# Optimization experiments

Measured on AMD Instinct MI355X. Metric: run time of the kernel, lower is better.

The kernel has to match this reference:

```python
import jax, jax.numpy as jnp
import numpy as np

PRED, TOTAL, ITEM = 100000, 120000, 100000
NUI = PRED + ITEM            # nodes in user2item / reverse-consumption graphs
NODES = TOTAL + ITEM         # embedding table rows
EMB = 64
EPS = 1e-5


def _gatv2(src, dst, x, Wl, bl, Wr, br, attn, n):
    """DGL GATv2Conv (1 head), activation=leaky_relu(0.01)."""
    fs = x @ Wl + bl                                   # fc_src
    fd = x @ Wr + br                                   # fc_dst
    e = jax.nn.leaky_relu(fs[src] + fd[dst], 0.2) @ attn   # [E_edges]
    m = jax.ops.segment_max(e, dst, n)                 # per-dst max (stable softmax)
    ex = jnp.exp(e - m[dst])
    denom = jax.ops.segment_sum(ex, dst, n)
    alpha = ex / denom[dst]                            # edge softmax over in-edges
    out = jax.ops.segment_sum(alpha[:, None] * fs[src], dst, n)
    return jax.nn.leaky_relu(out, 0.01)


def _bn(x, g, b):
    mu = jnp.mean(x, 0)
    var = jnp.var(x, 0)
    return (x - mu) * jax.lax.rsqrt(var + EPS) * g + b


def _mlp(x, W, b, g, beta):
    # Linear -> BatchNorm1d (train mode, batch stats) -> LeakyReLU(0.01)
    return jax.nn.leaky_relu(_bn(x @ W + b, g, beta), 0.01)


def _cheb(src, dst, x, W, b, lam, n):
    """ChebConv order-3: h = sum_k T_k(Lhat) x @ W_k + b, leaky_relu."""
    deg = jnp.clip(jax.ops.segment_sum(jnp.ones_like(dst, jnp.float32), dst, n), 1.0)
    dinv = jax.lax.rsqrt(deg)
    norm = dinv[src] * dinv[dst]                       # D^-1/2 A D^-1/2 edge weight

    def lhat(v):  # (2/lam)(I - Ahat) v - v
        av = jax.ops.segment_sum(norm[:, None] * v[src], dst, n)
        return (2.0 / lam) * (v - av) - v

    T0 = x
    T1 = lhat(T0)
    T2 = 2.0 * lhat(T1) - T0
    return jax.nn.leaky_relu(T0 @ W[0] + T1 @ W[1] + T2 @ W[2] + b, 0.01)


def setup_inputs() -> dict:
    key = jax.random.key(0)
    ks = jax.random.split(key, 24)
    ri = lambda k, n, hi: jax.random.randint(k, (n,), 0, hi, dtype=jnp.int32)
    rn = lambda k, shp, s=0.1: jax.random.normal(k, shp, jnp.float32) * s
    return {
        "emb": rn(ks[0], (NODES, EMB), 1.0),
        "bn0_g": jnp.ones((EMB,), jnp.float32),
        "bn0_b": jnp.zeros((EMB,), jnp.float32),
        "gat_Wl": rn(ks[1], (5, EMB, EMB)),
        "gat_bl": jnp.zeros((5, EMB), jnp.float32),
        "gat_Wr": rn(ks[2], (5, EMB, EMB)),
        "gat_br": jnp.zeros((5, EMB), jnp.float32),
        "gat_attn": rn(ks[3], (5, EMB)),
        "cheb_W": rn(ks[4], (3, EMB, EMB)),
        "cheb_b": jnp.zeros((EMB,), jnp.float32),
        "mlp_W": rn(ks[5], (5, 2 * EMB, EMB)),
        "mlp_b": jnp.zeros((5, EMB), jnp.float32),
        "mlp_g": jnp.ones((5, EMB), jnp.float32),
        "mlp_beta": jnp.zeros((5, EMB), jnp.float32),
        "lambda_max": jnp.array([2.0], jnp.float32),
        "u2i_src": ri(ks[6], 1500000, NUI),
        "u2i_dst": ri(ks[7], 1500000, NUI),
        "rc_src": ri(ks[8], 1500000, NUI),
        "rc_dst": ri(ks[9], 1500000, NUI),
        "i2u_src": ri(ks[10], 1000000, PRED),
        "i2u_dst": ri(ks[11], 1000000, PRED),
        "i2u_ids": jnp.arange(PRED, dtype=jnp.int32),
        "sn_src": ri(ks[12], 1000000, PRED),
        "sn_dst": ri(ks[13], 1000000, PRED),
        "snn_src": ri(ks[14], 1500000, TOTAL),
        "snn_dst": ri(ks[15], 1500000, TOTAL),
    }


def reference(emb, bn0_g, bn0_b, gat_Wl, gat_bl, gat_Wr, gat_br, gat_attn,
              cheb_W, cheb_b, mlp_W, mlp_b, mlp_g, mlp_beta, lambda_max,
              u2i_src, u2i_dst, rc_src, rc_dst, i2u_src, i2u_dst, i2u_ids,
              sn_src, sn_dst, snn_src, snn_dst):
    gat = lambda i, src, dst, x, n: _gatv2(src, dst, x, gat_Wl[i], gat_bl[i],
                                           gat_Wr[i], gat_br[i], gat_attn[i], n)
    mlp = lambda i, x: _mlp(x, mlp_W[i], mlp_b[i], mlp_g[i], mlp_beta[i])

    e = _bn(emb, bn0_g, bn0_b)                        # embedding_BN over all nodes
    pred_u = e[:PRED]
    total_u = e[:TOTAL]
    item_e = e[-ITEM:]
    uie = jnp.concatenate([pred_u, item_e], axis=0)   # [NUI, EMB]

    # --- spatial attention: item influence branch ---
    u2i_emb = gat(0, u2i_src, u2i_dst, uie, NUI)
    iie = gat(1, rc_src, rc_dst, u2i_emb, NUI)[:PRED]

    # --- spatial attention: social item branch ---
    su = uie[i2u_ids]                                 # embedding[_ID]
    i2u_emb = gat(2, i2u_src, i2u_dst, su, PRED)
    soc = uie[:PRED]                                  # embedding[social_g.nodes()]
    mask = (jnp.sum(i2u_emb, axis=1) != 0)[:, None]
    soc = soc.at[i2u_ids].set(jnp.where(mask, i2u_emb, soc[i2u_ids]))
    sie = gat(3, sn_src, sn_dst, soc, PRED)

    user_item_embed = mlp(0, jnp.concatenate([iie, sie], axis=1))

    # --- spectral attention ---
    lam = lambda_max[0]
    h = _cheb(snn_src, snn_dst, total_u, cheb_W, cheb_b, lam, TOTAL)
    h = _cheb(snn_src, snn_dst, h, cheb_W, cheb_b, lam, TOTAL)
    user_social_embed = gat(4, snn_src, snn_dst, h, TOTAL)[:PRED]

    # --- mutualistic layer ---
    h_uP = mlp(1, jnp.concatenate([user_item_embed, pred_u], axis=1))
    h_uS = mlp(2, jnp.concatenate([user_social_embed, pred_u], axis=1))
    h_m = h_uP * h_uS
    h_mP = jnp.concatenate([h_m * jax.nn.softmax(h_uP, axis=1), h_uP], axis=1)
    h_mS = jnp.concatenate([h_m * jax.nn.softmax(h_uS, axis=1), h_uS], axis=1)

    # --- prediction layer ---
    h_new_P = mlp(3, h_mP)
    h_new_S = mlp(4, h_mS)
    return (h_new_P, h_new_S)
```

## Files before the change

kernel.cpp:

```cpp
#include <hip/hip_runtime.h>
#include <math.h>

static const int PRED  = 100000;
static const int TOTAL = 120000;
static const int ITEM  = 100000;
static const int NUI   = PRED + ITEM;
static const int NODES = TOTAL + ITEM;
#define BN_EPS 1e-5f

__device__ inline float lrelu(float v, float s) { return v > 0.f ? v : s * v; }

__global__ void k_bn_stats(const float* __restrict__ x, int n, float* __restrict__ sums) {
  __shared__ float ls[256], ls2[256];
  int t = threadIdx.x;
  int col = t & 63;
  float s = 0.f, s2 = 0.f;
  for (int r = blockIdx.x * 4 + (t >> 6); r < n; r += gridDim.x * 4) {
    float v = x[(size_t)r * 64 + col];
    s += v; s2 += v * v;
  }
  ls[t] = s; ls2[t] = s2;
  __syncthreads();
  if (t < 64) {
    atomicAdd(&sums[t],      ls[t] + ls[t + 64] + ls[t + 128] + ls[t + 192]);
    atomicAdd(&sums[64 + t], ls2[t] + ls2[t + 64] + ls2[t + 128] + ls2[t + 192]);
  }
}

__global__ void k_bn_apply(const float* __restrict__ x, float* __restrict__ y,
                           const float* __restrict__ sums,
                           const float* __restrict__ g, const float* __restrict__ b,
                           int n, int relu) {
  size_t tot4 = (size_t)n * 16;
  size_t i = (size_t)blockIdx.x * blockDim.x + threadIdx.x;
  size_t st = (size_t)gridDim.x * blockDim.x;
  float inv_n = 1.f / (float)n;
  const float4* x4 = (const float4*)x;
  float4* y4 = (float4*)y;
  for (; i < tot4; i += st) {
    int c4 = (int)(i & 15) * 4;
    float4 v = x4[i];
    float4 o;
    #pragma unroll
    for (int j = 0; j < 4; ++j) {
      int c = c4 + j;
      float mean = sums[c] * inv_n;
      float var = fmaxf(sums[64 + c] * inv_n - mean * mean, 0.f);
      float vv = (j == 0) ? v.x : (j == 1) ? v.y : (j == 2) ? v.z : v.w;
      float oo = (vv - mean) * rsqrtf(var + BN_EPS) * g[c] + b[c];
      if (relu) oo = lrelu(oo, 0.01f);
      if (j == 0) o.x = oo; else if (j == 1) o.y = oo; else if (j == 2) o.z = oo; else o.w = oo;
    }
    y4[i] = o;
  }
}

__global__ void k_bn0_apply(const float* __restrict__ x, float* __restrict__ e_tot,
                            float* __restrict__ uie, const float* __restrict__ sums,
                            const float* __restrict__ g, const float* __restrict__ b) {
  size_t tot4 = (size_t)NODES * 16;
  size_t i = (size_t)blockIdx.x * blockDim.x + threadIdx.x;
  size_t st = (size_t)gridDim.x * blockDim.x;
  float inv_n = 1.f / (float)NODES;
  const float4* x4 = (const float4*)x;
  float4* e4 = (float4*)e_tot;
  float4* u4 = (float4*)uie;
  for (; i < tot4; i += st) {
    int c4 = (int)(i & 15) * 4;
    size_t row = i >> 4;
    float4 v = x4[i];
    float4 o;
    #pragma unroll
    for (int j = 0; j < 4; ++j) {
      int c = c4 + j;
      float mean = sums[c] * inv_n;
      float var = fmaxf(sums[64 + c] * inv_n - mean * mean, 0.f);
      float vv = (j == 0) ? v.x : (j == 1) ? v.y : (j == 2) ? v.z : v.w;
      float oo = (vv - mean) * rsqrtf(var + BN_EPS) * g[c] + b[c];
      if (j == 0) o.x = oo; else if (j == 1) o.y = oo; else if (j == 2) o.z = oo; else o.w = oo;
    }
    if (row < (size_t)TOTAL) e4[i] = o;
    else u4[((row - TOTAL) + PRED) * 16 + (i & 15)] = o;
    if (row < (size_t)PRED) u4[i] = o;
  }
}

__global__ __launch_bounds__(256) void k_gemm_dual(const float* __restrict__ A,
    const float* __restrict__ Wl, const float* __restrict__ bl,
    const float* __restrict__ Wr, const float* __restrict__ br,
    float* __restrict__ FS, float* __restrict__ FD, int n) {
  __shared__ float As[128][65];
  __shared__ float Ws[64][68];
  int t = threadIdx.x;
  int row0 = blockIdx.x * 128;
  for (int i = t; i < 2048; i += 256) {
    int r = i >> 4, c = (i & 15) * 4, gr = row0 + r;
    float4 a;
    if (gr < n) a = *(const float4*)&A[(size_t)gr * 64 + c];
    else { a.x = a.y = a.z = a.w = 0.f; }
    As[r][c] = a.x; As[r][c + 1] = a.y; As[r][c + 2] = a.z; As[r][c + 3] = a.w;
  }
  int cg = (t & 7) * 8;
  int rg = (t >> 3) * 4;
  for (int s = 0; s < 2; ++s) {
    const float* Wm = s ? Wr : Wl;
    const float* bias = s ? br : bl;
    __syncthreads();
    for (int i = t; i < 4096; i += 256) Ws[i >> 6][i & 63] = Wm[i];
    __syncthreads();
    float bb[8];
    *(float4*)&bb[0] = *(const float4*)&bias[cg];
    *(float4*)&bb[4] = *(const float4*)&bias[cg + 4];
    float acc[4][8];
    #pragma unroll
    for (int i = 0; i < 4; ++i)
      #pragma unroll
      for (int j = 0; j < 8; ++j) acc[i][j] = bb[j];
    for (int k = 0; k < 64; ++k) {
      float w[8], a[4];
      *(float4*)&w[0] = *(const float4*)&Ws[k][cg];
      *(float4*)&w[4] = *(const float4*)&Ws[k][cg + 4];
      #pragma unroll
      for (int i = 0; i < 4; ++i) a[i] = As[rg + i][k];
      #pragma unroll
      for (int i = 0; i < 4; ++i)
        #pragma unroll
        for (int j = 0; j < 8; ++j)
          acc[i][j] += a[i] * w[j];
    }
    float* C = s ? FD : FS;
    #pragma unroll
    for (int i = 0; i < 4; ++i) {
      int gr = row0 + rg + i;
      if (gr < n) {
        float4 o0, o1;
        o0.x = acc[i][0]; o0.y = acc[i][1]; o0.z = acc[i][2]; o0.w = acc[i][3];
        o1.x = acc[i][4]; o1.y = acc[i][5]; o1.z = acc[i][6]; o1.w = acc[i][7];
        *(float4*)&FS[0];
        *(float4*)&C[(size_t)gr * 64 + cg] = o0;
        *(float4*)&C[(size_t)gr * 64 + cg + 4] = o1;
      }
    }
  }
}

__global__ __launch_bounds__(256) void k_gemm_cat(const float* __restrict__ A1,
    const float* __restrict__ A2, const float* __restrict__ A3,
    const float* __restrict__ Wm, const float* __restrict__ bias,
    float* __restrict__ C, int n, int nseg, int relu, float* __restrict__ stats) {
  __shared__ float As[128][65];
  __shared__ float Ws[64][68];
  __shared__ float st[128];
  int t = threadIdx.x;
  int row0 = blockIdx.x * 128;
  int cg = (t & 7) * 8;
  int rg = (t >> 3) * 4;
  float bb[8];
  *(float4*)&bb[0] = *(const float4*)&bias[cg];
  *(float4*)&bb[4] = *(const float4*)&bias[cg + 4];
  float acc[4][8];
  #pragma unroll
  for (int i = 0; i < 4; ++i)
    #pragma unroll
    for (int j = 0; j < 8; ++j) acc[i][j] = bb[j];
  for (int s = 0; s < nseg; ++s) {
    const float* A = (s == 0) ? A1 : (s == 1) ? A2 : A3;
    __syncthreads();
    for (int i = t; i < 4096; i += 256) Ws[i >> 6][i & 63] = Wm[s * 4096 + i];
    for (int i = t; i < 2048; i += 256) {
      int r = i >> 4, c = (i & 15) * 4, gr = row0 + r;
      float4 a;
      if (gr < n) a = *(const float4*)&A[(size_t)gr * 64 + c];
      else { a.x = a.y = a.z = a.w = 0.f; }
      As[r][c] = a.x; As[r][c + 1] = a.y; As[r][c + 2] = a.z; As[r][c + 3] = a.w;
    }
    __syncthreads();
    for (int k = 0; k < 64; ++k) {
      float w[8], a[4];
      *(float4*)&w[0] = *(const float4*)&Ws[k][cg];
      *(float4*)&w[4] = *(const float4*)&Ws[k][cg + 4];
      #pragma unroll
      for (int i = 0; i < 4; ++i) a[i] = As[rg + i][k];
      #pragma unroll
      for (int i = 0; i < 4; ++i)
        #pragma unroll
        for (int j = 0; j < 8; ++j)
          acc[i][j] += a[i] * w[j];
    }
  }
  float csum[8], csq[8];
  #pragma unroll
  for (int j = 0; j < 8; ++j) { csum[j] = 0.f; csq[j] = 0.f; }
  #pragma unroll
  for (int i = 0; i < 4; ++i) {
    int gr = row0 + rg + i;
    if (gr < n) {
      #pragma unroll
      for (int j = 0; j < 8; ++j) {
        float o = acc[i][j];
        if (relu) o = lrelu(o, 0.01f);
        acc[i][j] = o;
        csum[j] += o;
        csq[j] += o * o;
      }
      float4 o0, o1;
      o0.x = acc[i][0]; o0.y = acc[i][1]; o0.z = acc[i][2]; o0.w = acc[i][3];
      o1.x = acc[i][4]; o1.y = acc[i][5]; o1.z = acc[i][6]; o1.w = acc[i][7];
      *(float4*)&C[(size_t)gr * 64 + cg] = o0;
      *(float4*)&C[(size_t)gr * 64 + cg + 4] = o1;
    }
  }
  if (stats) {
    __syncthreads();
    if (t < 128) st[t] = 0.f;
    __syncthreads();
    #pragma unroll
    for (int j = 0; j < 8; ++j) {
      atomicAdd(&st[cg + j], csum[j]);
      atomicAdd(&st[64 + cg + j], csq[j]);
    }
    __syncthreads();
    if (t < 128) atomicAdd(&stats[t], st[t]);
  }
}

__global__ __launch_bounds__(512) void k_bhist(const int* __restrict__ dst, int* __restrict__ M,
                                               int E, int nbuck, int chunk) {
  __shared__ int h[1600];
  int t = threadIdx.x, b = blockIdx.x;
  for (int k = t; k < nbuck; k += 512) h[k] = 0;
  __syncthreads();
  int beg = b * chunk, end = min(E, beg + chunk);
  for (int i = beg + t; i < end; i += 512) atomicAdd(&h[dst[i] >> 7], 1);
  __syncthreads();
  for (int k = t; k < nbuck; k += 512) M[k * 64 + b] = h[k];
}

__global__ void k_scan_part(const int* __restrict__ counts, int* __restrict__ bsums, int n) {
  __shared__ int sh[256];
  int t = threadIdx.x;
  int i = blockIdx.x * 256 + t;
  sh[t] = (i < n) ? counts[i] : 0;
  __syncthreads();
  for (int o = 128; o; o >>= 1) {
    if (t < o) sh[t] += sh[t + o];
    __syncthreads();
  }
  if (t == 0) bsums[blockIdx.x] = sh[0];
}

__global__ void k_scan_tops(int* __restrict__ bsums, int nb) {
  __shared__ int sh[256];
  int t = threadIdx.x;
  int carry = 0;
  for (int base = 0; base < nb; base += 256) {
    int i = base + t;
    int v = (i < nb) ? bsums[i] : 0;
    __syncthreads();
    sh[t] = v;
    __syncthreads();
    for (int o = 1; o < 256; o <<= 1) {
      int tv = (t >= o) ? sh[t - o] : 0;
      __syncthreads();
      sh[t] += tv;
      __syncthreads();
    }
    int incl = sh[t];
    int total = sh[255];
    if (i < nb) bsums[i] = incl - v + carry;
    carry += total;
  }
}

__global__ void k_scan_apply_ip(int* __restrict__ cnts, const int* __restrict__ bsums, int n) {
  __shared__ int sh[256];
  int t = threadIdx.x;
  int i = blockIdx.x * 256 + t;
  int v = (i < n) ? cnts[i] : 0;
  sh[t] = v;
  __syncthreads();
  for (int o = 1; o < 256; o <<= 1) {
    int tv = (t >= o) ? sh[t - o] : 0;
    __syncthreads();
    sh[t] += tv;
    __syncthreads();
  }
  if (i < n) cnts[i] = sh[t] - v + bsums[blockIdx.x];
}

__global__ __launch_bounds__(512) void k_bscatter(const int* __restrict__ src, const int* __restrict__ dst,
                                                  const int* __restrict__ M, unsigned int* __restrict__ tmp,
                                                  int E, int nbuck, int chunk) {
  __shared__ int cur[1600];
  int t = threadIdx.x, b = blockIdx.x;
  for (int k = t; k < nbuck; k += 512) cur[k] = M[k * 64 + b];
  __syncthreads();
  int beg = b * chunk, end = min(E, beg + chunk);
  for (int i = beg + t; i < end; i += 512) {
    int d = dst[i];
    int pos = atomicAdd(&cur[d >> 7], 1);
    tmp[pos] = ((unsigned int)(d & 127) << 25) | (unsigned int)src[i];
  }
}

__global__ __launch_bounds__(256) void k_bfinal(const unsigned int* __restrict__ tmp,
                                                const int* __restrict__ M,
                                                int* __restrict__ offs, int* __restrict__ csr,
                                                int E, int nbuck, int n,
                                                float* __restrict__ dinvOut) {
  __shared__ int h[128];
  int t = threadIdx.x, k = blockIdx.x;
  int base = M[k * 64];
  int next = (k + 1 < nbuck) ? M[(k + 1) * 64] : E;
  if (t < 128) h[t] = 0;
  __syncthreads();
  for (int i = base + t; i < next; i += 256) atomicAdd(&h[tmp[i] >> 25], 1);
  __syncthreads();
  if (t == 0) { int s = 0; for (int j = 0; j < 128; ++j) { int c = h[j]; h[j] = s; s += c; } }
  __syncthreads();
  int r0 = k << 7;
  int hstart = 0, hnext = 0;
  if (t < 128) {
    hstart = h[t];
    hnext = (t < 127) ? h[t + 1] : (next - base);
  }
  if (t < 128 && r0 + t < n) {
    offs[r0 + t] = base + hstart;
    if (dinvOut) dinvOut[r0 + t] = rsqrtf(fmaxf((float)(hnext - hstart), 1.f));
  }
  if (k == nbuck - 1 && t == 0) offs[n] = E;
  __syncthreads();
  for (int i = base + t; i < next; i += 256) {
    unsigned int v = tmp[i];
    int rl = (int)(v >> 25);
    int pos = base + atomicAdd(&h[rl], 1);
    csr[pos] = (int)(v & 0x01FFFFFFu);
  }
}

__global__ __launch_bounds__(256) void k_gat_fused(const float* __restrict__ fs,
                                                   const float* __restrict__ fd,
                                                   const float* __restrict__ attn,
                                                   const int* __restrict__ offs,
                                                   const int* __restrict__ csr_src,
                                                   const float* __restrict__ sel,
                                                   float* __restrict__ out, int n) {
  int lane = threadIdx.x & 63;
  int g  = lane >> 4;
  int li = lane & 15;
  int c4 = li * 4;
  int wid = (blockIdx.x * blockDim.x + threadIdx.x) >> 6;
  int nw = (gridDim.x * blockDim.x) >> 6;
  float4 ak = *(const float4*)&attn[c4];
  for (int r = wid; r < n; r += nw) {
    int beg = offs[r], end = offs[r + 1];
    float4 fdv = *(const float4*)&fd[(size_t)r * 64 + c4];
    float den = 0.f;
    float4 acc; acc.x = acc.y = acc.z = acc.w = 0.f;
    int e0 = beg + g;
    int s = (e0 < end) ? csr_src[e0] : 0;
    float4 f = *(const float4*)&fs[(size_t)s * 64 + c4];
    for (int e4 = beg; e4 < end; e4 += 4) {
      bool act = (e4 + g) < end;
      int en = e4 + 4 + g;
      int sn = (en < end) ? csr_src[en] : 0;
      float4 fn = *(const float4*)&fs[(size_t)sn * 64 + c4];
      float w = ak.x * lrelu(f.x + fdv.x, 0.2f)
              + ak.y * lrelu(f.y + fdv.y, 0.2f)
              + ak.z * lrelu(f.z + fdv.z, 0.2f)
              + ak.w * lrelu(f.w + fdv.w, 0.2f);
      w += __shfl_xor(w, 1);
      w += __shfl_xor(w, 2);
      w += __shfl_xor(w, 4);
      w += __shfl_xor(w, 8);
      float p = act ? __expf(w) : 0.f;
      den += p;
      acc.x += p * f.x;
      acc.y += p * f.y;
      acc.z += p * f.z;
      acc.w += p * f.w;
      s = sn; f = fn;
    }
    #pragma unroll
    for (int o = 16; o < 64; o <<= 1) {
      den   += __shfl_xor(den, o);
      acc.x += __shfl_xor(acc.x, o);
      acc.y += __shfl_xor(acc.y, o);
      acc.z += __shfl_xor(acc.z, o);
      acc.w += __shfl_xor(acc.w, o);
    }
    if (g == 0) {
      float inv = (end > beg) ? 1.f / den : 0.f;
      float4 o4;
      o4.x = lrelu(acc.x * inv, 0.01f);
      o4.y = lrelu(acc.y * inv, 0.01f);
      o4.z = lrelu(acc.z * inv, 0.01f);
      o4.w = lrelu(acc.w * inv, 0.01f);
      if (sel) {
        float rs = o4.x + o4.y + o4.z + o4.w;
        rs += __shfl_xor(rs, 1);
        rs += __shfl_xor(rs, 2);
        rs += __shfl_xor(rs, 4);
        rs += __shfl_xor(rs, 8);
        if (rs == 0.f) o4 = *(const float4*)&sel[(size_t)r * 64 + c4];
      }
      *(float4*)&out[(size_t)r * 64 + c4] = o4;
    }
  }
}

__global__ __launch_bounds__(256) void k_cheb_fused(const float* __restrict__ v,
                                                    const float* __restrict__ t0,
                                                    const float* __restrict__ dinv,
                                                    const int* __restrict__ offs,
                                                    const int* __restrict__ csr_src,
                                                    float* __restrict__ out,
                                                    const float* __restrict__ lamf,
                                                    int n, int mode) {
  int lane = threadIdx.x & 63;
  int g  = lane >> 4;
  int li = lane & 15;
  int c4 = li * 4;
  int wid = (blockIdx.x * blockDim.x + threadIdx.x) >> 6;
  int nw = (gridDim.x * blockDim.x) >> 6;
  float cc = 2.f / lamf[0];
  for (int r = wid; r < n; r += nw) {
    int beg = offs[r], end = offs[r + 1];
    float dr = dinv[r];
    float4 acc; acc.x = acc.y = acc.z = acc.w = 0.f;
    int e0 = beg + g;
    int s = (e0 < end) ? csr_src[e0] : 0;
    float ds = dinv[s];
    float4 f = *(const float4*)&v[(size_t)s * 64 + c4];
    for (int e4 = beg; e4 < end; e4 += 4) {
      bool act = (e4 + g) < end;
      int en = e4 + 4 + g;
      int sn = (en < end) ? csr_src[en] : 0;
      float dsn = dinv[sn];
      float4 fn = *(const float4*)&v[(size_t)sn * 64 + c4];
      float ns = act ? ds * dr : 0.f;
      acc.x += ns * f.x;
      acc.y += ns * f.y;
      acc.z += ns * f.z;
      acc.w += ns * f.w;
      s = sn; ds = dsn; f = fn;
    }
    #pragma unroll
    for (int o = 16; o < 64; o <<= 1) {
      acc.x += __shfl_xor(acc.x, o);
      acc.y += __shfl_xor(acc.y, o);
      acc.z += __shfl_xor(acc.z, o);
      acc.w += __shfl_xor(acc.w, o);
    }
    if (g == 0) {
      float4 vr = *(const float4*)&v[(size_t)r * 64 + c4];
      float4 o4;
      o4.x = cc * (vr.x - acc.x) - vr.x;
      o4.y = cc * (vr.y - acc.y) - vr.y;
      o4.z = cc * (vr.z - acc.z) - vr.z;
      o4.w = cc * (vr.w - acc.w) - vr.w;
      if (mode == 2) {
        float4 t = *(const float4*)&t0[(size_t)r * 64 + c4];
        o4.x = 2.f * o4.x - t.x;
        o4.y = 2.f * o4.y - t.y;
        o4.z = 2.f * o4.z - t.z;
        o4.w = 2.f * o4.w - t.w;
      }
      *(float4*)&out[(size_t)r * 64 + c4] = o4;
    }
  }
}

__global__ void k_softmax_mul(const float* __restrict__ a, const float* __restrict__ b,
                              float* __restrict__ out, int n) {
  int lane = threadIdx.x & 63;
  int wid = (blockIdx.x * blockDim.x + threadIdx.x) >> 6;
  int nw = (gridDim.x * blockDim.x) >> 6;
  for (int r = wid; r < n; r += nw) {
    size_t idx = (size_t)r * 64 + lane;
    float av = a[idx];
    float mx = av;
    for (int o = 32; o; o >>= 1) mx = fmaxf(mx, __shfl_xor(mx, o));
    float e = expf(av - mx);
    float s = e;
    for (int o = 32; o; o >>= 1) s += __shfl_xor(s, o);
    out[idx] = av * b[idx] * (e / s);
  }
}

extern "C" void kernel_launch(void* const* d_in, const int* in_sizes, int n_in,
                              void* d_out, int out_size, void* d_ws, size_t ws_size,
                              hipStream_t stream) {
  const float* emb      = (const float*)d_in[0];
  const float* bn0_g    = (const float*)d_in[1];
  const float* bn0_b    = (const float*)d_in[2];
  const float* gat_Wl   = (const float*)d_in[3];
  const float* gat_bl   = (const float*)d_in[4];
  const float* gat_Wr   = (const float*)d_in[5];
  const float* gat_br   = (const float*)d_in[6];
  const float* gat_attn = (const float*)d_in[7];
  const float* cheb_W   = (const float*)d_in[8];
  const float* cheb_b   = (const float*)d_in[9];
  const float* mlp_W    = (const float*)d_in[10];
  const float* mlp_b    = (const float*)d_in[11];
  const float* mlp_g    = (const float*)d_in[12];
  const float* mlp_beta = (const float*)d_in[13];
  const float* lam      = (const float*)d_in[14];
  const int* u2i_src = (const int*)d_in[15];
  const int* u2i_dst = (const int*)d_in[16];
  const int* rc_src  = (const int*)d_in[17];
  const int* rc_dst  = (const int*)d_in[18];
  const int* i2u_src = (const int*)d_in[19];
  const int* i2u_dst = (const int*)d_in[20];
  const int* sn_src  = (const int*)d_in[22];
  const int* sn_dst  = (const int*)d_in[23];
  const int* snn_src = (const int*)d_in[24];
  const int* snn_dst = (const int*)d_in[25];
  int E_u2i = in_sizes[15], E_rc = in_sizes[17], E_i2u = in_sizes[19];
  int E_sn = in_sizes[22], E_snn = in_sizes[24];

  float* Wp = (float*)d_ws;
  size_t off = 0;
  auto alloc = [&](size_t nf) { float* p = Wp + off; off += nf; return p; };
  float* e_tot = alloc((size_t)TOTAL * 64);
  float* POOL  = alloc((size_t)600000 * 64);
  int*   csr_src = (int*)alloc(1500000);
  int*   offs    = (int*)alloc(200064);
  float* spare   = alloc(200064);
  int*   bsums   = (int*)alloc(1024);
  float* dinv  = alloc(TOTAL);
  float* sums  = alloc(896);

  auto R = [&](size_t row) { return POOL + row * 64; };
  unsigned int* tmp_e = (unsigned int*)R(520000);
  int*          Mbuf  = (int*)R(545000);
  (void)spare;

  float* outP = (float*)d_out;
  float* outS = outP + (size_t)PRED * 64;

  auto build_csr = [&](const int* src, const int* dst, int E, int n, float* dv) {
    int nbuck = (n + 127) >> 7;
    int chunk = (E + 63) / 64;
    int L = nbuck * 64;
    int NB = (L + 255) / 256;
    k_bhist<<<64, 512, 0, stream>>>(dst, Mbuf, E, nbuck, chunk);
    k_scan_part<<<NB, 256, 0, stream>>>(Mbuf, bsums, L);
    k_scan_tops<<<1, 256, 0, stream>>>(bsums, NB);
    k_scan_apply_ip<<<NB, 256, 0, stream>>>(Mbuf, bsums, L);
    k_bscatter<<<64, 512, 0, stream>>>(src, dst, Mbuf, tmp_e, E, nbuck, chunk);
    k_bfinal<<<nbuck, 256, 0, stream>>>(tmp_e, Mbuf, offs, csr_src, E, nbuck, n, dv);
  };
  auto gat = [&](int i, const float* fs, const float* fd, int n, const float* sel, float* out) {
    k_gat_fused<<<(n + 3) / 4, 256, 0, stream>>>(fs, fd, gat_attn + i * 64, offs, csr_src, sel, out, n);
  };
  auto gat_gemms = [&](int i, const float* A, float* fs, float* fd, int n) {
    k_gemm_dual<<<(n + 127) / 128, 256, 0, stream>>>(A, gat_Wl + i * 4096, gat_bl + i * 64,
                                                     gat_Wr + i * 4096, gat_br + i * 64, fs, fd, n);
  };
  auto cat2s = [&](const float* A1, const float* A2, const float* Wm, const float* bias,
                   float* C, int n, int slot) {
    k_gemm_cat<<<(n + 127) / 128, 256, 0, stream>>>(A1, A2, nullptr, Wm, bias, C, n, 2, 0,
                                                    sums + slot * 128);
  };

  hipMemsetAsync(sums, 0, 896 * 4, stream);

  k_bn_stats<<<512, 256, 0, stream>>>(emb, NODES, sums);
  k_bn0_apply<<<2048, 256, 0, stream>>>(emb, e_tot, R(0), sums, bn0_g, bn0_b);

  build_csr(u2i_src, u2i_dst, E_u2i, NUI, nullptr);
  gat_gemms(0, R(0), R(200000), R(400000), NUI);
  gat(0, R(200000), R(400000), NUI, nullptr, R(0));

  build_csr(rc_src, rc_dst, E_rc, NUI, nullptr);
  gat_gemms(1, R(0), R(200000), R(400000), NUI);
  gat(1, R(200000), R(400000), NUI, nullptr, R(0));

  build_csr(i2u_src, i2u_dst, E_i2u, PRED, nullptr);
  gat_gemms(2, e_tot, R(200000), R(300000), PRED);
  gat(2, R(200000), R(300000), PRED, e_tot, R(400000));

  build_csr(sn_src, sn_dst, E_sn, PRED, nullptr);
  gat_gemms(3, R(400000), R(200000), R(500000), PRED);
  gat(3, R(200000), R(500000), PRED, nullptr, R(300000));

  cat2s(R(0), R(300000), mlp_W + 0 * 8192, mlp_b + 0, R(100000), PRED, 1);
  k_bn_apply<<<2048, 256, 0, stream>>>(R(100000), R(0), sums + 128, mlp_g + 0, mlp_beta + 0, PRED, 1);

  build_csr(snn_src, snn_dst, E_snn, TOTAL, dinv);

  auto cheb = [&](const float* T0, float* T1, float* T2, float* outC) {
    k_cheb_fused<<<(TOTAL + 3) / 4, 256, 0, stream>>>(T0, T0, dinv, offs, csr_src, T1, lam, TOTAL, 1);
    k_cheb_fused<<<(TOTAL + 3) / 4, 256, 0, stream>>>(T1, T0, dinv, offs, csr_src, T2, lam, TOTAL, 2);
    k_gemm_cat<<<(TOTAL + 127) / 128, 256, 0, stream>>>(T0, T1, T2, cheb_W, cheb_b, outC, TOTAL, 3, 1, nullptr);
  };
  cheb(e_tot, R(100000), R(220000), R(340000));
  cheb(R(340000), R(100000), R(220000), R(460000));

  gat_gemms(4, R(460000), R(100000), R(220000), TOTAL);
  gat(4, R(100000), R(220000), TOTAL, nullptr, R(460000));

  cat2s(R(0), e_tot, mlp_W + 1 * 8192, mlp_b + 64, R(100000), PRED, 2);
  k_bn_apply<<<2048, 256, 0, stream>>>(R(100000), R(100000), sums + 256, mlp_g + 64, mlp_beta + 64, PRED, 1);

  cat2s(R(460000), e_tot, mlp_W + 2 * 8192, mlp_b + 128, R(200000), PRED, 3);
  k_bn_apply<<<2048, 256, 0, stream>>>(R(200000), R(200000), sums + 384, mlp_g + 128, mlp_beta + 128, PRED, 1);

  k_softmax_mul<<<2048, 256, 0, stream>>>(R(100000), R(200000), R(300000), PRED);
  cat2s(R(300000), R(100000), mlp_W + 3 * 8192, mlp_b + 192, R(400000), PRED, 4);
  k_bn_apply<<<2048, 256, 0, stream>>>(R(400000), outP, sums + 512, mlp_g + 192, mlp_beta + 192, PRED, 1);

  k_softmax_mul<<<2048, 256, 0, stream>>>(R(200000), R(100000), R(300000), PRED);
  cat2s(R(300000), R(200000), mlp_W + 4 * 8192, mlp_b + 256, R(400000), PRED, 5);
  k_bn_apply<<<2048, 256, 0, stream>>>(R(400000), outS, sums + 640, mlp_g + 256, mlp_beta + 256, PRED, 1);
}
```

Measured before the change: 2.049 ms.

## Widen per-lane features in GAT/Cheb gathers and merge CSR scan into one kernel

The GAT and Chebyshev gather kernels now give each lane 8 features instead of 4, so a wavefront processes 8 edges per step instead of 4 and the shuffle reduction shrinks. The three-kernel prefix scan used in CSR construction is replaced by a single 1024-thread block scan built on wave shuffles, which cuts launches. Smaller edits switch leaky ReLU to fmaxf, use __expf in the softmax-multiply kernel, remove a dead load, and inline the cheb lambda. The trade-off is more registers per lane and a serial single-block scan.

```diff
diff --git a/kernel.cpp b/kernel.cpp
--- a/kernel.cpp
+++ b/kernel.cpp
@@ -8,7 +8,7 @@
 static const int NODES = TOTAL + ITEM;
 #define BN_EPS 1e-5f
 
-__device__ inline float lrelu(float v, float s) { return v > 0.f ? v : s * v; }
+__device__ inline float lrelu(float v, float s) { return fmaxf(v, s * v); }
 
 __global__ void k_bn_stats(const float* __restrict__ x, int n, float* __restrict__ sums) {
   __shared__ float ls[256], ls2[256];
@@ -136,7 +136,6 @@
         float4 o0, o1;
         o0.x = acc[i][0]; o0.y = acc[i][1]; o0.z = acc[i][2]; o0.w = acc[i][3];
         o1.x = acc[i][4]; o1.y = acc[i][5]; o1.z = acc[i][6]; o1.w = acc[i][7];
-        *(float4*)&FS[0];
         *(float4*)&C[(size_t)gr * 64 + cg] = o0;
         *(float4*)&C[(size_t)gr * 64 + cg + 4] = o1;
       }
@@ -224,6 +223,23 @@
   }
 }
 
+__global__ void k_softmax_mul(const float* __restrict__ a, const float* __restrict__ b,
+                              float* __restrict__ out, int n) {
+  int lane = threadIdx.x & 63;
+  int wid = (blockIdx.x * blockDim.x + threadIdx.x) >> 6;
+  int nw = (gridDim.x * blockDim.x) >> 6;
+  for (int r = wid; r < n; r += nw) {
+    size_t idx = (size_t)r * 64 + lane;
+    float av = a[idx];
+    float mx = av;
+    for (int o = 32; o; o >>= 1) mx = fmaxf(mx, __shfl_xor(mx, o));
+    float e = __expf(av - mx);
+    float s = e;
+    for (int o = 32; o; o >>= 1) s += __shfl_xor(s, o);
+    out[idx] = av * b[idx] * (e / s);
+  }
+}
+
 __global__ __launch_bounds__(512) void k_bhist(const int* __restrict__ dst, int* __restrict__ M,
                                                int E, int nbuck, int chunk) {
   __shared__ int h[1600];
@@ -236,56 +252,33 @@
   for (int k = t; k < nbuck; k += 512) M[k * 64 + b] = h[k];
 }
 
-__global__ void k_scan_part(const int* __restrict__ counts, int* __restrict__ bsums, int n) {
-  __shared__ int sh[256];
-  int t = threadIdx.x;
-  int i = blockIdx.x * 256 + t;
-  sh[t] = (i < n) ? counts[i] : 0;
-  __syncthreads();
-  for (int o = 128; o; o >>= 1) {
-    if (t < o) sh[t] += sh[t + o];
-    __syncthreads();
-  }
-  if (t == 0) bsums[blockIdx.x] = sh[0];
-}
-
-__global__ void k_scan_tops(int* __restrict__ bsums, int nb) {
-  __shared__ int sh[256];
-  int t = threadIdx.x;
-  int carry = 0;
-  for (int base = 0; base < nb; base += 256) {
+__global__ __launch_bounds__(1024) void k_scan_one(int* __restrict__ cnts, int L) {
+  __shared__ int wsum[16];
+  __shared__ int carry_s;
+  int t = threadIdx.x, lane = t & 63, w = t >> 6;
+  if (t == 0) carry_s = 0;
+  __syncthreads();
+  for (int base = 0; base < L; base += 1024) {
     int i = base + t;
-    int v = (i < nb) ? bsums[i] : 0;
-    __syncthreads();
-    sh[t] = v;
-    __syncthreads();
-    for (int o = 1; o < 256; o <<= 1) {
-      int tv = (t >= o) ? sh[t - o] : 0;
-      __syncthreads();
-      sh[t] += tv;
-      __syncthreads();
-    }
-    int incl = sh[t];
-    int total = sh[255];
-    if (i < nb) bsums[i] = incl - v + carry;
-    carry += total;
-  }
-}
-
-__global__ void k_scan_apply_ip(int* __restrict__ cnts, const int* __restrict__ bsums, int n) {
-  __shared__ int sh[256];
-  int t = threadIdx.x;
-  int i = blockIdx.x * 256 + t;
-  int v = (i < n) ? cnts[i] : 0;
-  sh[t] = v;
-  __syncthreads();
-  for (int o = 1; o < 256; o <<= 1) {
-    int tv = (t >= o) ? sh[t - o] : 0;
-    __syncthreads();
-    sh[t] += tv;
-    __syncthreads();
-  }
-  if (i < n) cnts[i] = sh[t] - v + bsums[blockIdx.x];
+    int v = (i < L) ? cnts[i] : 0;
+    int x = v;
+    #pragma unroll
+    for (int o = 1; o < 64; o <<= 1) {
+      int y = __shfl_up(x, o);
+      if (lane >= o) x += y;
+    }
+    if (lane == 63) wsum[w] = x;
+    __syncthreads();
+    int carry = carry_s;
+    int wadd = 0;
+    #pragma unroll
+    for (int j = 0; j < 16; ++j) { int sv = wsum[j]; if (j < w) wadd += sv; }
+    int incl = x + wadd + carry;
+    if (i < L) cnts[i] = incl - v;
+    __syncthreads();
+    if (t == 1023) carry_s = incl;
+    __syncthreads();
+  }
 }
 
 __global__ __launch_bounds__(512) void k_bscatter(const int* __restrict__ src, const int* __restrict__ dst,
@@ -346,65 +339,74 @@
                                                    const float* __restrict__ sel,
                                                    float* __restrict__ out, int n) {
   int lane = threadIdx.x & 63;
-  int g  = lane >> 4;
-  int li = lane & 15;
-  int c4 = li * 4;
+  int g  = lane >> 3;
+  int c8 = (lane & 7) * 8;
   int wid = (blockIdx.x * blockDim.x + threadIdx.x) >> 6;
   int nw = (gridDim.x * blockDim.x) >> 6;
-  float4 ak = *(const float4*)&attn[c4];
+  float4 ak0 = *(const float4*)&attn[c8];
+  float4 ak1 = *(const float4*)&attn[c8 + 4];
   for (int r = wid; r < n; r += nw) {
     int beg = offs[r], end = offs[r + 1];
-    float4 fdv = *(const float4*)&fd[(size_t)r * 64 + c4];
+    float4 fd0 = *(const float4*)&fd[(size_t)r * 64 + c8];
+    float4 fd1 = *(const float4*)&fd[(size_t)r * 64 + c8 + 4];
     float den = 0.f;
-    float4 acc; acc.x = acc.y = acc.z = acc.w = 0.f;
+    float4 a0, a1;
+    a0.x = a0.y = a0.z = a0.w = 0.f;
+    a1.x = a1.y = a1.z = a1.w = 0.f;
     int e0 = beg + g;
     int s = (e0 < end) ? csr_src[e0] : 0;
-    float4 f = *(const float4*)&fs[(size_t)s * 64 + c4];
-    for (int e4 = beg; e4 < end; e4 += 4) {
-      bool act = (e4 + g) < end;
-      int en = e4 + 4 + g;
+    float4 f0 = *(const float4*)&fs[(size_t)s * 64 + c8];
+    float4 f1 = *(const float4*)&fs[(size_t)s * 64 + c8 + 4];
+    for (int e8 = beg; e8 < end; e8 += 8) {
+      bool act = (e8 + g) < end;
+      int en = e8 + 8 + g;
       int sn = (en < end) ? csr_src[en] : 0;
-      float4 fn = *(const float4*)&fs[(size_t)sn * 64 + c4];
-      float w = ak.x * lrelu(f.x + fdv.x, 0.2f)
-              + ak.y * lrelu(f.y + fdv.y, 0.2f)
-              + ak.z * lrelu(f.z + fdv.z, 0.2f)
-              + ak.w * lrelu(f.w + fdv.w, 0.2f);
+      float4 p0 = *(const float4*)&fs[(size_t)sn * 64 + c8];
+      float4 p1 = *(const float4*)&fs[(size_t)sn * 64 + c8 + 4];
+      float w = ak0.x * lrelu(f0.x + fd0.x, 0.2f)
+              + ak0.y * lrelu(f0.y + fd0.y, 0.2f)
+              + ak0.z * lrelu(f0.z + fd0.z, 0.2f)
+              + ak0.w * lrelu(f0.w + fd0.w, 0.2f)
+              + ak1.x * lrelu(f1.x + fd1.x, 0.2f)
+              + ak1.y * lrelu(f1.y + fd1.y, 0.2f)
+              + ak1.z * lrelu(f1.z + fd1.z, 0.2f)
+              + ak1.w * lrelu(f1.w + fd1.w, 0.2f);
       w += __shfl_xor(w, 1);
       w += __shfl_xor(w, 2);
       w += __shfl_xor(w, 4);
-      w += __shfl_xor(w, 8);
       float p = act ? __expf(w) : 0.f;
       den += p;
-      acc.x += p * f.x;
-      acc.y += p * f.y;
-      acc.z += p * f.z;
-      acc.w += p * f.w;
-      s = sn; f = fn;
-    }
-    #pragma unroll
-    for (int o = 16; o < 64; o <<= 1) {
-      den   += __shfl_xor(den, o);
-      acc.x += __shfl_xor(acc.x, o);
-      acc.y += __shfl_xor(acc.y, o);
-      acc.z += __shfl_xor(acc.z, o);
-      acc.w += __shfl_xor(acc.w, o);
+      a0.x += p * f0.x; a0.y += p * f0.y; a0.z += p * f0.z; a0.w += p * f0.w;
+      a1.x += p * f1.x; a1.y += p * f1.y; a1.z += p * f1.z; a1.w += p * f1.w;
+      s = sn; f0 = p0; f1 = p1;
+    }
+    #pragma unroll
+    for (int o = 8; o < 64; o <<= 1) {
+      den  += __shfl_xor(den, o);
+      a0.x += __shfl_xor(a0.x, o); a0.y += __shfl_xor(a0.y, o);
+      a0.z += __shfl_xor(a0.z, o); a0.w += __shfl_xor(a0.w, o);
+      a1.x += __shfl_xor(a1.x, o); a1.y += __shfl_xor(a1.y, o);
+      a1.z += __shfl_xor(a1.z, o); a1.w += __shfl_xor(a1.w, o);
     }
     if (g == 0) {
       float inv = (end > beg) ? 1.f / den : 0.f;
-      float4 o4;
-      o4.x = lrelu(acc.x * inv, 0.01f);
-      o4.y = lrelu(acc.y * inv, 0.01f);
-      o4.z = lrelu(acc.z * inv, 0.01f);
-      o4.w = lrelu(acc.w * inv, 0.01f);
+      float4 o0, o1;
+      o0.x = lrelu(a0.x * inv, 0.01f); o0.y = lrelu(a0.y * inv, 0.01f);
+      o0.z = lrelu(a0.z * inv, 0.01f); o0.w = lrelu(a0.w * inv, 0.01f);
+      o1.x = lrelu(a1.x * inv, 0.01f); o1.y = lrelu(a1.y * inv, 0.01f);
+      o1.z = lrelu(a1.z * inv, 0.01f); o1.w = lrelu(a1.w * inv, 0.01f);
       if (sel) {
-        float rs = o4.x + o4.y + o4.z + o4.w;
+        float rs = o0.x + o0.y + o0.z + o0.w + o1.x + o1.y + o1.z + o1.w;
         rs += __shfl_xor(rs, 1);
         rs += __shfl_xor(rs, 2);
         rs += __shfl_xor(rs, 4);
-        rs += __shfl_xor(rs, 8);
-        if (rs == 0.f) o4 = *(const float4*)&sel[(size_t)r * 64 + c4];
+        if (rs == 0.f) {
+          o0 = *(const float4*)&sel[(size_t)r * 64 + c8];
+          o1 = *(const float4*)&sel[(size_t)r * 64 + c8 + 4];
+        }
       }
-      *(float4*)&out[(size_t)r * 64 + c4] = o4;
+      *(float4*)&out[(size_t)r * 64 + c8] = o0;
+      *(float4*)&out[(size_t)r * 64 + c8 + 4] = o1;
     }
   }
 }
@@ -418,73 +420,60 @@
                                                     const float* __restrict__ lamf,
                                                     int n, int mode) {
   int lane = threadIdx.x & 63;
-  int g  = lane >> 4;
-  int li = lane & 15;
-  int c4 = li * 4;
+  int g  = lane >> 3;
+  int c8 = (lane & 7) * 8;
   int wid = (blockIdx.x * blockDim.x + threadIdx.x) >> 6;
   int nw = (gridDim.x * blockDim.x) >> 6;
   float cc = 2.f / lamf[0];
   for (int r = wid; r < n; r += nw) {
     int beg = offs[r], end = offs[r + 1];
     float dr = dinv[r];
-    float4 acc; acc.x = acc.y = acc.z = acc.w = 0.f;
+    float4 a0, a1;
+    a0.x = a0.y = a0.z = a0.w = 0.f;
+    a1.x = a1.y = a1.z = a1.w = 0.f;
     int e0 = beg + g;
     int s = (e0 < end) ? csr_src[e0] : 0;
     float ds = dinv[s];
-    float4 f = *(const float4*)&v[(size_t)s * 64 + c4];
-    for (int e4 = beg; e4 < end; e4 += 4) {
-      bool act = (e4 + g) < end;
-      int en = e4 + 4 + g;
+    float4 f0 = *(const float4*)&v[(size_t)s * 64 + c8];
+    float4 f1 = *(const float4*)&v[(size_t)s * 64 + c8 + 4];
+    for (int e8 = beg; e8 < end; e8 += 8) {
+      bool act = (e8 + g) < end;
+      int en = e8 + 8 + g;
       int sn = (en < end) ? csr_src[en] : 0;
       float dsn = dinv[sn];
-      float4 fn = *(const float4*)&v[(size_t)sn * 64 + c4];
+      float4 p0 = *(const float4*)&v[(size_t)sn * 64 + c8];
+      float4 p1 = *(const float4*)&v[(size_t)sn * 64 + c8 + 4];
       float ns = act ? ds * dr : 0.f;
-      acc.x += ns * f.x;
-      acc.y += ns * f.y;
-      acc.z += ns * f.z;
-      acc.w += ns * f.w;
-      s = sn; ds = dsn; f = fn;
-    }
-    #pragma unroll
-    for (int o = 16; o < 64; o <<= 1) {
-      acc.x += __shfl_xor(acc.x, o);
-      acc.y += __shfl_xor(acc.y, o);
-      acc.z += __shfl_xor(acc.z, o);
-      acc.w += __shfl_xor(acc.w, o);
+      a0.x += ns * f0.x; a0.y += ns * f0.y; a0.z += ns * f0.z; a0.w += ns * f0.w;
+      a1.x += ns * f1.x; a1.y += ns * f1.y; a1.z += ns * f1.z; a1.w += ns * f1.w;
+      s = sn; ds = dsn; f0 = p0; f1 = p1;
+    }
+    #pragma unroll
+    for (int o = 8; o < 64; o <<= 1) {
+      a0.x += __shfl_xor(a0.x, o); a0.y += __shfl_xor(a0.y, o);
+      a0.z += __shfl_xor(a0.z, o); a0.w += __shfl_xor(a0.w, o);
+      a1.x += __shfl_xor(a1.x, o); a1.y += __shfl_xor(a1.y, o);
+      a1.z += __shfl_xor(a1.z, o); a1.w += __shfl_xor(a1.w, o);
     }
     if (g == 0) {
-      float4 vr = *(const float4*)&v[(size_t)r * 64 + c4];
-      float4 o4;
-      o4.x = cc * (vr.x - acc.x) - vr.x;
-      o4.y = cc * (vr.y - acc.y) - vr.y;
-      o4.z = cc * (vr.z - acc.z) - vr.z;
-      o4.w = cc * (vr.w - acc.w) - vr.w;
+      float4 v0 = *(const float4*)&v[(size_t)r * 64 + c8];
+      float4 v1 = *(const float4*)&v[(size_t)r * 64 + c8 + 4];
+      float4 o0, o1;
+      o0.x = cc * (v0.x - a0.x) - v0.x; o0.y = cc * (v0.y - a0.y) - v0.y;
+      o0.z = cc * (v0.z - a0.z) - v0.z; o0.w = cc * (v0.w - a0.w) - v0.w;
+      o1.x = cc * (v1.x - a1.x) - v1.x; o1.y = cc * (v1.y - a1.y) - v1.y;
+      o1.z = cc * (v1.z - a1.z) - v1.z; o1.w = cc * (v1.w - a1.w) - v1.w;
       if (mode == 2) {
-        float4 t = *(const float4*)&t0[(size_t)r * 64 + c4];
-        o4.x = 2.f * o4.x - t.x;
-        o4.y = 2.f * o4.y - t.y;
-        o4.z = 2.f * o4.z - t.z;
-        o4.w = 2.f * o4.w - t.w;
+        float4 t0a = *(const float4*)&t0[(size_t)r * 64 + c8];
+        float4 t0b = *(const float4*)&t0[(size_t)r * 64 + c8 + 4];
+        o0.x = 2.f * o0.x - t0a.x; o0.y = 2.f * o0.y - t0a.y;
+        o0.z = 2.f * o0.z - t0a.z; o0.w = 2.f * o0.w - t0a.w;
+        o1.x = 2.f * o1.x - t0b.x; o1.y = 2.f * o1.y - t0b.y;
+        o1.z = 2.f * o1.z - t0b.z; o1.w = 2.f * o1.w - t0b.w;
       }
-      *(float4*)&out[(size_t)r * 64 + c4] = o4;
-    }
-  }
-}
-
-__global__ void k_softmax_mul(const float* __restrict__ a, const float* __restrict__ b,
-                              float* __restrict__ out, int n) {
-  int lane = threadIdx.x & 63;
-  int wid = (blockIdx.x * blockDim.x + threadIdx.x) >> 6;
-  int nw = (gridDim.x * blockDim.x) >> 6;
-  for (int r = wid; r < n; r += nw) {
-    size_t idx = (size_t)r * 64 + lane;
-    float av = a[idx];
-    float mx = av;
-    for (int o = 32; o; o >>= 1) mx = fmaxf(mx, __shfl_xor(mx, o));
-    float e = expf(av - mx);
-    float s = e;
-    for (int o = 32; o; o >>= 1) s += __shfl_xor(s, o);
-    out[idx] = av * b[idx] * (e / s);
+      *(float4*)&out[(size_t)r * 64 + c8] = o0;
+      *(float4*)&out[(size_t)r * 64 + c8 + 4] = o1;
+    }
   }
 }
 
@@ -530,11 +519,10 @@
   int*   bsums   = (int*)alloc(1024);
   float* dinv  = alloc(TOTAL);
   float* sums  = alloc(896);
-
   auto R = [&](size_t row) { return POOL + row * 64; };
   unsigned int* tmp_e = (unsigned int*)R(520000);
   int*          Mbuf  = (int*)R(545000);
-  (void)spare;
+  (void)spare; (void)bsums;
 
   float* outP = (float*)d_out;
   float* outS = outP + (size_t)PRED * 64;
@@ -543,11 +531,8 @@
     int nbuck = (n + 127) >> 7;
     int chunk = (E + 63) / 64;
     int L = nbuck * 64;
-    int NB = (L + 255) / 256;
     k_bhist<<<64, 512, 0, stream>>>(dst, Mbuf, E, nbuck, chunk);
-    k_scan_part<<<NB, 256, 0, stream>>>(Mbuf, bsums, L);
-    k_scan_tops<<<1, 256, 0, stream>>>(bsums, NB);
-    k_scan_apply_ip<<<NB, 256, 0, stream>>>(Mbuf, bsums, L);
+    k_scan_one<<<1, 1024, 0, stream>>>(Mbuf, L);
     k_bscatter<<<64, 512, 0, stream>>>(src, dst, Mbuf, tmp_e, E, nbuck, chunk);
     k_bfinal<<<nbuck, 256, 0, stream>>>(tmp_e, Mbuf, offs, csr_src, E, nbuck, n, dv);
   };
@@ -590,13 +575,14 @@
 
   build_csr(snn_src, snn_dst, E_snn, TOTAL, dinv);
 
-  auto cheb = [&](const float* T0, float* T1, float* T2, float* outC) {
-    k_cheb_fused<<<(TOTAL + 3) / 4, 256, 0, stream>>>(T0, T0, dinv, offs, csr_src, T1, lam, TOTAL, 1);
-    k_cheb_fused<<<(TOTAL + 3) / 4, 256, 0, stream>>>(T1, T0, dinv, offs, csr_src, T2, lam, TOTAL, 2);
-    k_gemm_cat<<<(TOTAL + 127) / 128, 256, 0, stream>>>(T0, T1, T2, cheb_W, cheb_b, outC, TOTAL, 3, 1, nullptr);
-  };
-  cheb(e_tot, R(100000), R(220000), R(340000));
-  cheb(R(340000), R(100000), R(220000), R(460000));
+  k_cheb_fused<<<(TOTAL + 3) / 4, 256, 0, stream>>>(e_tot, e_tot, dinv, offs, csr_src, R(100000), lam, TOTAL, 1);
+  k_cheb_fused<<<(TOTAL + 3) / 4, 256, 0, stream>>>(R(100000), e_tot, dinv, offs, csr_src, R(220000), lam, TOTAL, 2);
+  k_gemm_cat<<<(TOTAL + 127) / 128, 256, 0, stream>>>(e_tot, R(100000), R(220000), cheb_W, cheb_b,
+                                                      R(340000), TOTAL, 3, 1, nullptr);
+  k_cheb_fused<<<(TOTAL + 3) / 4, 256, 0, stream>>>(R(340000), R(340000), dinv, offs, csr_src, R(100000), lam, TOTAL, 1);
+  k_cheb_fused<<<(TOTAL + 3) / 4, 256, 0, stream>>>(R(100000), R(340000), dinv, offs, csr_src, R(220000), lam, TOTAL, 2);
+  k_gemm_cat<<<(TOTAL + 127) / 128, 256, 0, stream>>>(R(340000), R(100000), R(220000), cheb_W, cheb_b,
+                                                      R(460000), TOTAL, 3, 1, nullptr);
 
   gat_gemms(4, R(460000), R(100000), R(220000), TOTAL);
   gat(4, R(100000), R(220000), TOTAL, nullptr, R(460000));
```

New measurement: 2.287 ms. +11.6%, slower.
